# Kernel optimization log

Hardware: AMD Instinct MI355X
Metric: run time of the kernel (lower is better)

The kernel has to match this reference:

```python
import jax, jax.numpy as jnp
import numpy as np

H = 8  # n_heads

def setup_inputs() -> dict:
    key = jax.random.key(0)
    ks = jax.random.split(key, 7)
    B, G, D, KD, E = 16, 1024, 512, 64, 512  # batch, graph_size, input_dim, key_dim=embed//H, embed_dim
    q = jax.random.normal(ks[0], (B * G, D), jnp.float32)
    mask = jax.random.bernoulli(ks[1], 0.15, (B, G))  # True = padded node
    s_in = 1.0 / np.sqrt(D)
    Wq = jax.random.uniform(ks[2], (KD, D), jnp.float32, -s_in, s_in)
    Wk = jax.random.uniform(ks[3], (KD, D), jnp.float32, -s_in, s_in)
    Wv = jax.random.uniform(ks[4], (KD, D), jnp.float32, -s_in, s_in)
    s_o = 1.0 / np.sqrt(KD)
    Wout_w = jax.random.uniform(ks[5], (E, KD), jnp.float32, -s_o, s_o)
    Wout_b = jax.random.uniform(ks[6], (E,), jnp.float32, -1.0 / np.sqrt(E), 1.0 / np.sqrt(E))
    return {"q": q, "mask": mask, "Wq": Wq, "Wk": Wk, "Wv": Wv,
            "Wout_w": Wout_w, "Wout_b": Wout_b, "graph_size": G}


def reference(q, mask, Wq, Wk, Wv, Wout_w, Wout_b, graph_size):
    G = graph_size
    B = q.shape[0] // G
    KD = Wq.shape[0]
    norm = 1.0 / jnp.sqrt(jnp.asarray(KD, jnp.float32))
    # torch .view(n_heads, B, G, -1) on a (B*G, KD) tensor: row-major reshape
    Q = (q @ Wq.T).reshape(H, B, G, -1)  # per-head dim = KD // H
    K = (q @ Wk.T).reshape(H, B, G, -1)
    V = (q @ Wv.T).reshape(H, B, G, -1)
    compat = norm * jnp.einsum('hbqd,hbkd->hbqk', Q, K)  # (H,B,G,G)
    m = mask[None, :, None, :]  # broadcast == repeat over query dim and heads
    compat = jnp.where(m, jnp.float32(-30.0), compat)  # evaluate=False path
    attn = jax.nn.softmax(compat, axis=-1)
    attn = jnp.where(m, jnp.float32(0.0), attn)  # second mask fill
    heads = jnp.einsum('hbqk,hbkd->hbqd', attn, V)  # (H,B,G,KD//H)
    # permute(1,2,0,3) then flatten heads -> (B*G, H*(KD//H)=KD)
    out = heads.transpose(1, 2, 0, 3).reshape(B * G, -1) @ Wout_w.T + Wout_b
    return out
```

## Files before the change

### kernel.cpp

```cpp
#include <hip/hip_runtime.h>
#include <hip/hip_bf16.h>

#define NROWS 16384
#define DDIM  512
#define KDIM  64
#define EDIM  512
#define GSZ   1024
#define BSZ   16
#define HSZ   8

typedef float f32x16 __attribute__((ext_vector_type(16)));
typedef short bf16x8 __attribute__((ext_vector_type(8)));

union FragU { uint u[4]; uint4 u4; bf16x8 s; };

static __device__ __forceinline__ float fexp2(float x) {
  return __builtin_amdgcn_exp2f(x);
}
static __device__ __forceinline__ uint bf16r(float x) {
  const uint u = __builtin_bit_cast(uint, x);
  return (u + 0x7FFFu + ((u >> 16) & 1u)) >> 16;
}
static __device__ __forceinline__ uint cvtpk(float lo, float hi) {
  return (bf16r(lo) & 0xFFFFu) | (bf16r(hi) << 16);
}
static __device__ __forceinline__ uint apk(float lo, float hi) {
  uint r;
  asm("v_cvt_pk_bf16_f32 %0, %1, %2" : "=v"(r) : "v"(lo), "v"(hi));
  return r;
}
static __device__ __forceinline__ uint pk2e(float a, float b) {
  const uint lo = __builtin_bit_cast(uint, fexp2(a)) + 0x8000u;
  const uint hi = __builtin_bit_cast(uint, fexp2(b)) + 0x8000u;
  return __builtin_amdgcn_perm(hi, lo, 0x07060302u);
}
static __device__ __forceinline__ void plswap(uint& a, uint& b) {
  auto r = __builtin_amdgcn_permlane32_swap(a, b, false, false);
  a = r[0]; b = r[1];
}
static __device__ __forceinline__ void plswapf(float& a, float& b) {
  uint au = __builtin_bit_cast(uint, a), bu = __builtin_bit_cast(uint, b);
  plswap(au, bu);
  a = __builtin_bit_cast(float, au); b = __builtin_bit_cast(float, bu);
}
static __device__ __forceinline__ uint vperm16(uint a, uint b, int d1) {
  const uint lo = d1 ? (a >> 16) : (a & 0xFFFFu);
  const uint hi = d1 ? (b >> 16) : (b & 0xFFFFu);
  return lo | (hi << 16);
}

__global__ __launch_bounds__(256) void k_mask2(const void* __restrict__ mraw,
                                               uint* __restrict__ mbu) {
  __shared__ int flags[2];
  const int tid = threadIdx.x;
  if (tid < 2) flags[tid] = 0;
  __syncthreads();
  const unsigned int* u = (const unsigned int*)mraw;
  int bad = 0, isf = 0;
  for (int i = tid; i < 4096; i += 256) {
    const unsigned v = u[i];
    bad |= (v > 1u) ? 1 : 0;
    isf |= (v == 0x3F800000u) ? 1 : 0;
  }
  if (bad) flags[0] = 1;
  if (isf) flags[1] = 1;
  __syncthreads();
  const int fmt = flags[1] ? 2 : (flags[0] ? 1 : 0);
  const int b = blockIdx.x;
  const uint maskedw = cvtpk(-1e30f, 0.0f);
  for (int g = tid; g < GSZ; g += 256) {
    const int idx = b * GSZ + g;
    bool m;
    if (fmt == 0)      m = ((const int*)mraw)[idx] != 0;
    else if (fmt == 1) m = ((const unsigned char*)mraw)[idx] != 0;
    else               m = ((const float*)mraw)[idx] != 0.0f;
    mbu[idx] = m ? maskedw : 0u;
  }
}

__global__ __launch_bounds__(384) void k_qkv2(const float* __restrict__ q,
    const float* __restrict__ Wq, const float* __restrict__ Wk,
    const float* __restrict__ Wv,
    ushort* __restrict__ Qbf, ushort* __restrict__ Kbf, ushort* __restrict__ Vbf) {
  __shared__ uint4 lds_a[16 * 64];
  __shared__ uint4 lds_w[16 * 192];
  const int tid = threadIdx.x;
  const int rowbase = blockIdx.x * 64;
  const int w = tid >> 6, lane = tid & 63, hi = lane >> 5, ln = lane & 31;
  const int wr = (w < 3) ? 0 : 1;
  const int wc = (w < 3) ? w : (w - 3);

  f32x16 acc0, acc1;
#pragma unroll
  for (int j = 0; j < 16; ++j) { acc0[j] = 0.0f; acc1[j] = 0.0f; }

#pragma unroll 1
  for (int ch = 0; ch < 4; ++ch) {
    const int k0 = ch * 128;
    __syncthreads();
#pragma unroll 1
    for (int ep = tid; ep < 512; ep += 384) {
      const int row = ep >> 3, sp = ep & 7;
      const float* src = q + (size_t)(rowbase + row) * DDIM + k0 + sp * 16;
      const float4 f0 = *(const float4*)(src);
      const float4 f1 = *(const float4*)(src + 4);
      const float4 f2 = *(const float4*)(src + 8);
      const float4 f3 = *(const float4*)(src + 12);
      uint4 w0, w1;
      w0.x = apk(f0.x, f0.y); w0.y = apk(f0.z, f0.w);
      w0.z = apk(f1.x, f1.y); w0.w = apk(f1.z, f1.w);
      w1.x = apk(f2.x, f2.y); w1.y = apk(f2.z, f2.w);
      w1.z = apk(f3.x, f3.y); w1.w = apk(f3.z, f3.w);
      const int sl0 = sp * 2, sl1 = sp * 2 + 1;
      lds_a[sl0 * 64 + (row ^ (sl0 & 7))] = w0;
      lds_a[sl1 * 64 + (row ^ (sl1 & 7))] = w1;
    }
#pragma unroll 1
    for (int ep = tid; ep < 1536; ep += 384) {
      const int c = ep >> 3, sp = ep & 7;
      const float* wsrc = (c < 64) ? (Wq + (size_t)c * DDIM)
                        : (c < 128) ? (Wk + (size_t)(c - 64) * DDIM)
                                    : (Wv + (size_t)(c - 128) * DDIM);
      const float* src = wsrc + k0 + sp * 16;
      const float4 f0 = *(const float4*)(src);
      const float4 f1 = *(const float4*)(src + 4);
      const float4 f2 = *(const float4*)(src + 8);
      const float4 f3 = *(const float4*)(src + 12);
      uint4 w0, w1;
      w0.x = apk(f0.x, f0.y); w0.y = apk(f0.z, f0.w);
      w0.z = apk(f1.x, f1.y); w0.w = apk(f1.z, f1.w);
      w1.x = apk(f2.x, f2.y); w1.y = apk(f2.z, f2.w);
      w1.z = apk(f3.x, f3.y); w1.w = apk(f3.z, f3.w);
      const int sl0 = sp * 2, sl1 = sp * 2 + 1;
      lds_w[sl0 * 192 + (c ^ (sl0 & 7))] = w0;
      lds_w[sl1 * 192 + (c ^ (sl1 & 7))] = w1;
    }
    __syncthreads();
#pragma unroll
    for (int kc8 = 0; kc8 < 8; ++kc8) {
      const int sl = kc8 * 2 + hi;
      FragU aq, b0, b1;
      aq.u4 = lds_a[sl * 64 + ((wr * 32 + ln) ^ (sl & 7))];
      b0.u4 = lds_w[sl * 192 + ((wc * 64 + ln) ^ (sl & 7))];
      b1.u4 = lds_w[sl * 192 + ((wc * 64 + 32 + ln) ^ (sl & 7))];
      acc0 = __builtin_amdgcn_mfma_f32_32x32x16_bf16(aq.s, b0.s, acc0, 0, 0, 0);
      acc1 = __builtin_amdgcn_mfma_f32_32x32x16_bf16(aq.s, b1.s, acc1, 0, 0, 0);
    }
  }

  constexpr float QS = 0.125f * 1.44269504088896340736f;
  ushort* dst = (wc == 0) ? Qbf : (wc == 1) ? Kbf : Vbf;
  const float scale = (wc == 0) ? QS : 1.0f;
#pragma unroll
  for (int j = 0; j < 16; ++j) {
    const int row = rowbase + wr * 32 + (j & 3) + 8 * (j >> 2) + 4 * hi;
    dst[(size_t)row * 64 + ln]      = (ushort)bf16r(acc0[j] * scale);
    dst[(size_t)row * 64 + 32 + ln] = (ushort)bf16r(acc1[j] * scale);
  }
}

__global__ __launch_bounds__(256) void k_attn6(const ushort* __restrict__ Qbf,
    const ushort* __restrict__ Kbf, const ushort* __restrict__ Vbf,
    const uint* __restrict__ mbu, float* __restrict__ Hm) {
  __shared__ __align__(16) uint4  KL[1024];
  __shared__ uint                 MB[1024];
  __shared__ __align__(16) ushort VT[8 * 1040];
  const int tid = threadIdx.x;
  const int b = blockIdx.y, h = blockIdx.z;
  const size_t hb = ((size_t)h * 2048 + (size_t)b * 128) * 64;

#pragma unroll
  for (int i = 0; i < 4; ++i) {
    const int tt = tid + i * 256;
    KL[tt] = *(const uint4*)(&Kbf[hb + (size_t)tt * 8]);
    MB[tt] = mbu[b * GSZ + tt];
  }
#pragma unroll
  for (int i = 0; i < 2; ++i) {
    const int t = (tid + i * 256) * 2;
    const uint4 v0 = *(const uint4*)(&Vbf[hb + (size_t)t * 8]);
    const uint4 v1 = *(const uint4*)(&Vbf[hb + (size_t)(t + 1) * 8]);
    const uint* ap = (const uint*)&v0;
    const uint* cp = (const uint*)&v1;
#pragma unroll
    for (int d = 0; d < 8; ++d)
      *(uint*)&VT[d * 1040 + t] = vperm16(ap[d >> 1], cp[d >> 1], d & 1);
  }

  const int w = tid >> 6, lane = tid & 63, hi = lane >> 5, ln = lane & 31;
  const int q = (blockIdx.x * 4 + w) * 32 + ln;

  FragU bq;
  if (hi == 0) {
    bq.u4 = *(const uint4*)(&Qbf[hb + (size_t)q * 8]);
  } else {
    bq.u[0] = 0x00003F80u; bq.u[1] = 0; bq.u[2] = 0; bq.u[3] = 0;
  }
  __syncthreads();

  f32x16 acc;
#pragma unroll
  for (int j = 0; j < 16; ++j) acc[j] = 0.0f;
  f32x16 zero;
#pragma unroll
  for (int j = 0; j < 16; ++j) zero[j] = 0.0f;

  const ushort* vbase = VT + ln * 1040;

#pragma unroll 2
  for (int kt = 0; kt < 32; ++kt) {
    const int tok = kt * 32 + ln;
    FragU ka;
    if (hi == 0) {
      ka.u4 = KL[tok];
    } else {
      ka.u[0] = MB[tok]; ka.u[1] = 0; ka.u[2] = 0; ka.u[3] = 0;
    }
    FragU va0, va1;
    if (ln < 8) {
      va0.u4 = *(const uint4*)(vbase + kt * 32 + hi * 8);
      va1.u4 = *(const uint4*)(vbase + kt * 32 + 16 + hi * 8);
    } else if (ln == 8) {
      va0.u[0] = va0.u[1] = va0.u[2] = va0.u[3] = 0x3F803F80u;
      va1.u4 = va0.u4;
    } else {
      va0.u[0] = va0.u[1] = va0.u[2] = va0.u[3] = 0;
      va1.u4 = va0.u4;
    }

    f32x16 s = __builtin_amdgcn_mfma_f32_32x32x16_bf16(ka.s, bq.s, zero, 0, 0, 0);

    uint x0 = pk2e(s[0], s[1]),   x1 = pk2e(s[2], s[3]);
    uint y0 = pk2e(s[4], s[5]),   y1 = pk2e(s[6], s[7]);
    uint x2 = pk2e(s[8], s[9]),   x3 = pk2e(s[10], s[11]);
    uint y2 = pk2e(s[12], s[13]), y3 = pk2e(s[14], s[15]);
    plswap(x0, y0);
    plswap(x1, y1);
    plswap(x2, y2);
    plswap(x3, y3);
    FragU pa;  pa.u[0] = x0;  pa.u[1] = x1;  pa.u[2] = y0;  pa.u[3] = y1;
    FragU pb;  pb.u[0] = x2;  pb.u[1] = x3;  pb.u[2] = y2;  pb.u[3] = y3;

    acc = __builtin_amdgcn_mfma_f32_32x32x16_bf16(va0.s, pa.s, acc, 0, 0, 0);
    acc = __builtin_amdgcn_mfma_f32_32x32x16_bf16(va1.s, pb.s, acc, 0, 0, 0);
  }

  float la = acc[4], lb = acc[4];
  plswapf(la, lb);
  const float inv = (la > 0.0f) ? 1.0f / la : 0.0f;
  float* op = Hm + ((size_t)b * GSZ + q) * 64 + h * 8 + hi * 4;
  *(float4*)op = make_float4(acc[0] * inv, acc[1] * inv, acc[2] * inv, acc[3] * inv);
}

__global__ __launch_bounds__(256) void k_out2(const float* __restrict__ Hm,
    const float* __restrict__ Ww, const float* __restrict__ Wb,
    float* __restrict__ out) {
  __shared__ uint4 lds_h[8 * 128];
  __shared__ uint4 lds_e[8 * 128];
  const int tid = threadIdx.x;
  const int colbase = blockIdx.x * 128;
  const int rowbase = blockIdx.y * 128;
  const int w = tid >> 6, lane = tid & 63, hi = lane >> 5, ln = lane & 31;
  const int wr = w >> 1, wc = w & 1;

#pragma unroll
  for (int i = 0; i < 2; ++i) {
    const int ep = tid + i * 256;
    const int row = ep >> 2, sp = ep & 3;
    const float* src = Hm + (size_t)(rowbase + row) * 64 + sp * 16;
    const float4 f0 = *(const float4*)(src);
    const float4 f1 = *(const float4*)(src + 4);
    const float4 f2 = *(const float4*)(src + 8);
    const float4 f3 = *(const float4*)(src + 12);
    uint4 w0, w1;
    w0.x = apk(f0.x, f0.y); w0.y = apk(f0.z, f0.w);
    w0.z = apk(f1.x, f1.y); w0.w = apk(f1.z, f1.w);
    w1.x = apk(f2.x, f2.y); w1.y = apk(f2.z, f2.w);
    w1.z = apk(f3.x, f3.y); w1.w = apk(f3.z, f3.w);
    const int sl0 = sp * 2, sl1 = sp * 2 + 1;
    lds_h[sl0 * 128 + (row ^ (sl0 & 7))] = w0;
    lds_h[sl1 * 128 + (row ^ (sl1 & 7))] = w1;
  }
#pragma unroll
  for (int i = 0; i < 2; ++i) {
    const int ep = tid + i * 256;
    const int c = ep >> 2, sp = ep & 3;
    const float* src = Ww + (size_t)(colbase + c) * 64 + sp * 16;
    const float4 f0 = *(const float4*)(src);
    const float4 f1 = *(const float4*)(src + 4);
    const float4 f2 = *(const float4*)(src + 8);
    const float4 f3 = *(const float4*)(src + 12);
    uint4 w0, w1;
    w0.x = apk(f0.x, f0.y); w0.y = apk(f0.z, f0.w);
    w0.z = apk(f1.x, f1.y); w0.w = apk(f1.z, f1.w);
    w1.x = apk(f2.x, f2.y); w1.y = apk(f2.z, f2.w);
    w1.z = apk(f3.x, f3.y); w1.w = apk(f3.z, f3.w);
    const int sl0 = sp * 2, sl1 = sp * 2 + 1;
    lds_e[sl0 * 128 + (c ^ (sl0 & 7))] = w0;
    lds_e[sl1 * 128 + (c ^ (sl1 & 7))] = w1;
  }
  __syncthreads();

  f32x16 a00, a01, a10, a11;
#pragma unroll
  for (int j = 0; j < 16; ++j) { a00[j] = 0.0f; a01[j] = 0.0f; a10[j] = 0.0f; a11[j] = 0.0f; }

#pragma unroll
  for (int kc8 = 0; kc8 < 4; ++kc8) {
    const int sl = kc8 * 2 + hi;
    FragU fa0, fa1, fb0, fb1;
    fa0.u4 = lds_h[sl * 128 + ((wr * 64 + ln) ^ (sl & 7))];
    fa1.u4 = lds_h[sl * 128 + ((wr * 64 + 32 + ln) ^ (sl & 7))];
    fb0.u4 = lds_e[sl * 128 + ((wc * 64 + ln) ^ (sl & 7))];
    fb1.u4 = lds_e[sl * 128 + ((wc * 64 + 32 + ln) ^ (sl & 7))];
    a00 = __builtin_amdgcn_mfma_f32_32x32x16_bf16(fa0.s, fb0.s, a00, 0, 0, 0);
    a01 = __builtin_amdgcn_mfma_f32_32x32x16_bf16(fa0.s, fb1.s, a01, 0, 0, 0);
    a10 = __builtin_amdgcn_mfma_f32_32x32x16_bf16(fa1.s, fb0.s, a10, 0, 0, 0);
    a11 = __builtin_amdgcn_mfma_f32_32x32x16_bf16(fa1.s, fb1.s, a11, 0, 0, 0);
  }

  const float bias0 = Wb[colbase + wc * 64 + ln];
  const float bias1 = Wb[colbase + wc * 64 + 32 + ln];
  const int col0 = colbase + wc * 64 + ln;
#pragma unroll
  for (int j = 0; j < 16; ++j) {
    const int r0 = rowbase + wr * 64 + (j & 3) + 8 * (j >> 2) + 4 * hi;
    out[(size_t)r0 * EDIM + col0]            = a00[j] + bias0;
    out[(size_t)r0 * EDIM + col0 + 32]       = a01[j] + bias1;
    out[(size_t)(r0 + 32) * EDIM + col0]      = a10[j] + bias0;
    out[(size_t)(r0 + 32) * EDIM + col0 + 32] = a11[j] + bias1;
  }
}

extern "C" void kernel_launch(void* const* d_in, const int* in_sizes, int n_in,
                              void* d_out, int out_size, void* d_ws, size_t ws_size,
                              hipStream_t stream) {
  const float* q    = (const float*)d_in[0];
  const void*  mask = d_in[1];
  const float* Wq   = (const float*)d_in[2];
  const float* Wk   = (const float*)d_in[3];
  const float* Wv   = (const float*)d_in[4];
  const float* Ww   = (const float*)d_in[5];
  const float* Wb   = (const float*)d_in[6];

  float* ws = (float*)d_ws;
  float* Hm    = ws;
  uint*  mbu   = (uint*)(Hm + (size_t)NROWS * KDIM);
  ushort* Qbf  = (ushort*)(mbu + 16384);
  ushort* Kbf  = Qbf + (size_t)NROWS * KDIM;
  ushort* Vbf  = Kbf + (size_t)NROWS * KDIM;

  k_mask2<<<BSZ, 256, 0, stream>>>(mask, mbu);
  k_qkv2<<<NROWS / 64, 384, 0, stream>>>(q, Wq, Wk, Wv, Qbf, Kbf, Vbf);
  k_attn6<<<dim3(8, BSZ, HSZ), 256, 0, stream>>>(Qbf, Kbf, Vbf, mbu, Hm);
  k_out2<<<dim3(EDIM / 128, NROWS / 128), 256, 0, stream>>>(Hm, Ww, Wb, (float*)d_out);
}
```

Before: 69.77 us.

## Apply key mask via zeroed V columns and ones row instead of score bias

The padding mask is no longer added to the scores through an extra K/Q mfma slot. Instead masked keys have their V values zeroed and their denominator ones-row entry cleared, and V is stored in LDS with a permuted token order so the exp-packed probabilities line up without permlane32 swaps. The inner loop becomes branch-free, with pointer-stepped LDS loads, and the Q fragment's upper half now reads real data against a zeroed K row. This removes per-iteration permlane swaps and the divergent fragment setup. In exchange, exp is computed for masked keys, which relies on unmasked scores staying bounded.

Result: faster. 62.63 us (-10.2%).

```diff
diff --git a/kernel.cpp b/kernel.cpp
--- a/kernel.cpp
+++ b/kernel.cpp
@@ -21,9 +21,6 @@
   const uint u = __builtin_bit_cast(uint, x);
   return (u + 0x7FFFu + ((u >> 16) & 1u)) >> 16;
 }
-static __device__ __forceinline__ uint cvtpk(float lo, float hi) {
-  return (bf16r(lo) & 0xFFFFu) | (bf16r(hi) << 16);
-}
 static __device__ __forceinline__ uint apk(float lo, float hi) {
   uint r;
   asm("v_cvt_pk_bf16_f32 %0, %1, %2" : "=v"(r) : "v"(lo), "v"(hi));
@@ -49,8 +46,9 @@
   return lo | (hi << 16);
 }
 
-__global__ __launch_bounds__(256) void k_mask2(const void* __restrict__ mraw,
-                                               uint* __restrict__ mbu) {
+__global__ __launch_bounds__(256) void k_mask3(const void* __restrict__ mraw,
+                                               uint* __restrict__ onesw,
+                                               uint* __restrict__ vmw) {
   __shared__ int flags[2];
   const int tid = threadIdx.x;
   if (tid < 2) flags[tid] = 0;
@@ -67,14 +65,20 @@
   __syncthreads();
   const int fmt = flags[1] ? 2 : (flags[0] ? 1 : 0);
   const int b = blockIdx.x;
-  const uint maskedw = cvtpk(-1e30f, 0.0f);
-  for (int g = tid; g < GSZ; g += 256) {
-    const int idx = b * GSZ + g;
-    bool m;
-    if (fmt == 0)      m = ((const int*)mraw)[idx] != 0;
-    else if (fmt == 1) m = ((const unsigned char*)mraw)[idx] != 0;
-    else               m = ((const float*)mraw)[idx] != 0.0f;
-    mbu[idx] = m ? maskedw : 0u;
+  for (int pair = tid; pair < 512; pair += 256) {
+    const int g0 = b * GSZ + pair * 2;
+    bool m0, m1;
+    if (fmt == 0) {
+      m0 = ((const int*)mraw)[g0] != 0;  m1 = ((const int*)mraw)[g0 + 1] != 0;
+    } else if (fmt == 1) {
+      m0 = ((const unsigned char*)mraw)[g0] != 0;
+      m1 = ((const unsigned char*)mraw)[g0 + 1] != 0;
+    } else {
+      m0 = ((const float*)mraw)[g0] != 0.0f;
+      m1 = ((const float*)mraw)[g0 + 1] != 0.0f;
+    }
+    onesw[b * 512 + pair] = (m0 ? 0u : 0x3F80u) | (m1 ? 0u : 0x3F800000u);
+    vmw[b * 512 + pair]   = (m0 ? 0u : 0xFFFFu) | (m1 ? 0u : 0xFFFF0000u);
   }
 }
 
@@ -159,12 +163,12 @@
   }
 }
 
-__global__ __launch_bounds__(256) void k_attn6(const ushort* __restrict__ Qbf,
+__global__ __launch_bounds__(256) void k_attn7(const ushort* __restrict__ Qbf,
     const ushort* __restrict__ Kbf, const ushort* __restrict__ Vbf,
-    const uint* __restrict__ mbu, float* __restrict__ Hm) {
-  __shared__ __align__(16) uint4  KL[1024];
-  __shared__ uint                 MB[1024];
-  __shared__ __align__(16) ushort VT[8 * 1040];
+    const uint* __restrict__ onesw, const uint* __restrict__ vmw,
+    float* __restrict__ Hm) {
+  __shared__ __align__(16) uint4  KL[1025];
+  __shared__ __align__(16) ushort VT[9 * 1040];
   const int tid = threadIdx.x;
   const int b = blockIdx.y, h = blockIdx.z;
   const size_t hb = ((size_t)h * 2048 + (size_t)b * 128) * 64;
@@ -173,29 +177,34 @@
   for (int i = 0; i < 4; ++i) {
     const int tt = tid + i * 256;
     KL[tt] = *(const uint4*)(&Kbf[hb + (size_t)tt * 8]);
-    MB[tt] = mbu[b * GSZ + tt];
+  }
+  if (tid == 0) {
+    uint4 z; z.x = 0; z.y = 0; z.z = 0; z.w = 0;
+    KL[1024] = z;
   }
 #pragma unroll
   for (int i = 0; i < 2; ++i) {
-    const int t = (tid + i * 256) * 2;
+    const int pair = tid + i * 256;
+    const int t = pair * 2;
+    const uint ow = onesw[b * 512 + pair];
+    const uint vm = vmw[b * 512 + pair];
     const uint4 v0 = *(const uint4*)(&Vbf[hb + (size_t)t * 8]);
     const uint4 v1 = *(const uint4*)(&Vbf[hb + (size_t)(t + 1) * 8]);
     const uint* ap = (const uint*)&v0;
     const uint* cp = (const uint*)&v1;
+    const int s = t & 15;
+    const int c = (t & ~15) | (s & 3) | ((s & 4) << 1) | ((s & 8) >> 1);
 #pragma unroll
     for (int d = 0; d < 8; ++d)
-      *(uint*)&VT[d * 1040 + t] = vperm16(ap[d >> 1], cp[d >> 1], d & 1);
+      *(uint*)&VT[d * 1040 + c] = vperm16(ap[d >> 1], cp[d >> 1], d & 1) & vm;
+    *(uint*)&VT[8 * 1040 + c] = ow;
   }
 
   const int w = tid >> 6, lane = tid & 63, hi = lane >> 5, ln = lane & 31;
   const int q = (blockIdx.x * 4 + w) * 32 + ln;
 
   FragU bq;
-  if (hi == 0) {
-    bq.u4 = *(const uint4*)(&Qbf[hb + (size_t)q * 8]);
-  } else {
-    bq.u[0] = 0x00003F80u; bq.u[1] = 0; bq.u[2] = 0; bq.u[3] = 0;
-  }
+  bq.u4 = *(const uint4*)(&Qbf[hb + (size_t)q * 8]);
   __syncthreads();
 
   f32x16 acc;
@@ -205,41 +214,26 @@
 #pragma unroll
   for (int j = 0; j < 16; ++j) zero[j] = 0.0f;
 
-  const ushort* vbase = VT + ln * 1040;
+  const char* kptr = (const char*)KL + (hi ? 1024 * 16 : ln * 16);
+  const int kstep = hi ? 0 : 512;
+  const ushort* vptr = VT + (ln < 8 ? ln : 8) * 1040 + hi * 8;
 
 #pragma unroll 2
   for (int kt = 0; kt < 32; ++kt) {
-    const int tok = kt * 32 + ln;
-    FragU ka;
-    if (hi == 0) {
-      ka.u4 = KL[tok];
-    } else {
-      ka.u[0] = MB[tok]; ka.u[1] = 0; ka.u[2] = 0; ka.u[3] = 0;
-    }
-    FragU va0, va1;
-    if (ln < 8) {
-      va0.u4 = *(const uint4*)(vbase + kt * 32 + hi * 8);
-      va1.u4 = *(const uint4*)(vbase + kt * 32 + 16 + hi * 8);
-    } else if (ln == 8) {
-      va0.u[0] = va0.u[1] = va0.u[2] = va0.u[3] = 0x3F803F80u;
-      va1.u4 = va0.u4;
-    } else {
-      va0.u[0] = va0.u[1] = va0.u[2] = va0.u[3] = 0;
-      va1.u4 = va0.u4;
-    }
+    FragU ka, va0, va1;
+    ka.u4  = *(const uint4*)kptr;
+    va0.u4 = *(const uint4*)(vptr);
+    va1.u4 = *(const uint4*)(vptr + 16);
+    kptr += kstep;
+    vptr += 32;
 
     f32x16 s = __builtin_amdgcn_mfma_f32_32x32x16_bf16(ka.s, bq.s, zero, 0, 0, 0);
 
-    uint x0 = pk2e(s[0], s[1]),   x1 = pk2e(s[2], s[3]);
-    uint y0 = pk2e(s[4], s[5]),   y1 = pk2e(s[6], s[7]);
-    uint x2 = pk2e(s[8], s[9]),   x3 = pk2e(s[10], s[11]);
-    uint y2 = pk2e(s[12], s[13]), y3 = pk2e(s[14], s[15]);
-    plswap(x0, y0);
-    plswap(x1, y1);
-    plswap(x2, y2);
-    plswap(x3, y3);
-    FragU pa;  pa.u[0] = x0;  pa.u[1] = x1;  pa.u[2] = y0;  pa.u[3] = y1;
-    FragU pb;  pb.u[0] = x2;  pb.u[1] = x3;  pb.u[2] = y2;  pb.u[3] = y3;
+    FragU pa, pb;
+    pa.u[0] = pk2e(s[0], s[1]);   pa.u[1] = pk2e(s[2], s[3]);
+    pa.u[2] = pk2e(s[4], s[5]);   pa.u[3] = pk2e(s[6], s[7]);
+    pb.u[0] = pk2e(s[8], s[9]);   pb.u[1] = pk2e(s[10], s[11]);
+    pb.u[2] = pk2e(s[12], s[13]); pb.u[3] = pk2e(s[14], s[15]);
 
     acc = __builtin_amdgcn_mfma_f32_32x32x16_bf16(va0.s, pa.s, acc, 0, 0, 0);
     acc = __builtin_amdgcn_mfma_f32_32x32x16_bf16(va1.s, pb.s, acc, 0, 0, 0);
@@ -345,13 +339,14 @@
 
   float* ws = (float*)d_ws;
   float* Hm    = ws;
-  uint*  mbu   = (uint*)(Hm + (size_t)NROWS * KDIM);
-  ushort* Qbf  = (ushort*)(mbu + 16384);
+  uint*  onesw = (uint*)(Hm + (size_t)NROWS * KDIM);
+  uint*  vmw   = onesw + BSZ * 512;
+  ushort* Qbf  = (ushort*)(vmw + BSZ * 512);
   ushort* Kbf  = Qbf + (size_t)NROWS * KDIM;
   ushort* Vbf  = Kbf + (size_t)NROWS * KDIM;
 
-  k_mask2<<<BSZ, 256, 0, stream>>>(mask, mbu);
+  k_mask3<<<BSZ, 256, 0, stream>>>(mask, onesw, vmw);
   k_qkv2<<<NROWS / 64, 384, 0, stream>>>(q, Wq, Wk, Wv, Qbf, Kbf, Vbf);
-  k_attn6<<<dim3(8, BSZ, HSZ), 256, 0, stream>>>(Qbf, Kbf, Vbf, mbu, Hm);
+  k_attn7<<<dim3(8, BSZ, HSZ), 256, 0, stream>>>(Qbf, Kbf, Vbf, onesw, vmw, Hm);
   k_out2<<<dim3(EDIM / 128, NROWS / 128), 256, 0, stream>>>(Hm, Ww, Wb, (float*)d_out);
 }
```
